# Kernel optimization log

Hardware: AMD Instinct MI355X
Metric: run time of the kernel (lower is better)

## Reference

```python
import jax, jax.numpy as jnp
import numpy as np

D = 64  # max disparity search range (d in the torch module)


def setup_inputs() -> dict:
    key = jax.random.key(0)
    k1, k2 = jax.random.split(key)
    B, C, H, W = 8, 128, 128, 256
    x1 = jax.random.normal(k1, (B, C, H, W), dtype=jnp.float32)
    x2 = jax.random.normal(k2, (B, C, H, W), dtype=jnp.float32)
    return {"x1": x1, "x2": x2}


def _corr_volume(x1, x2, d):
    # result[n, i, h, w] = (1/C) * sum_c x1[n,c,h,w] * x2[n,c,h,w-i], zero where w-i < 0
    n, c, h, w = x2.shape
    slices = []
    for i in range(d + 1):
        # shift x2 right by i columns, zero-padding on the left
        shifted = jnp.pad(x2[:, :, :, : w - i] if i > 0 else x2,
                          ((0, 0), (0, 0), (0, 0), (i, 0)))
        slices.append(jnp.sum(x1 * shifted, axis=1))  # [n, h, w]
    cv = jnp.stack(slices, axis=1)  # [n, d+1, h, w]
    return cv * (1.0 / c)


def reference(x1, x2):
    return _corr_volume(x1, x2, D)
```

## Files before the change

### kernel.cpp

```cpp
#include <hip/hip_runtime.h>
#include <hip/hip_fp16.h>


constexpr int B   = 8;
constexpr int C   = 128;
constexpr int H   = 128;
constexpr int W   = 256;
constexpr int NI  = 65;
constexpr int HW  = H * W;
constexpr int CHW = C * HW;
constexpr int KC2 = 8;
constexpr int X2W = 320;
constexpr int NCHUNK = C / (2 * KC2);

typedef _Float16 half2v __attribute__((ext_vector_type(2)));

__device__ inline unsigned int pack2(float a, float b) {
    __half2 h = __floats2half2_rn(a, b);
    return __builtin_bit_cast(unsigned int, h);
}

__device__ inline float fdot2f(unsigned int a, unsigned int b, float c) {
#if __has_builtin(__builtin_amdgcn_fdot2)
    return __builtin_amdgcn_fdot2(__builtin_bit_cast(half2v, a),
                                  __builtin_bit_cast(half2v, b), c, false);
#else
    __half2 ha = __builtin_bit_cast(__half2, a);
    __half2 hb = __builtin_bit_cast(__half2, b);
    float2 fa = __half22float2(ha), fb = __half22float2(hb);
    return fmaf(fa.x, fb.x, fmaf(fa.y, fb.y, c));
#endif
}

__global__ __launch_bounds__(512, 4)
void corr_volume_kernel(const float* __restrict__ x1,
                        const float* __restrict__ x2,
                        float* __restrict__ out) {
    const int bh  = blockIdx.x;
    const int n   = blockIdx.y;
    const int tid = threadIdx.x;
    const int l   = tid & 63;
    const int q   = tid >> 6;
    const int hsel = q >> 2;
    const int qi   = q & 3;

    __shared__ unsigned int x1h[2][KC2][W];
    __shared__ unsigned int x2h[2][KC2][X2W];

    float acc[16][4];
    #pragma unroll
    for (int il = 0; il < 16; ++il)
        #pragma unroll
        for (int wl = 0; wl < 4; ++wl) acc[il][wl] = 0.0f;
    float acc64[4] = {0.f, 0.f, 0.f, 0.f};

    const int j0a = 4 * l - 16 * qi + 48;

    const float* x1b = x1 + n * CHW + (2 * bh) * W;
    const float* x2b = x2 + n * CHW + (2 * bh) * W;

    if (tid < 256) {
        const int hh = tid >> 7;
        const int r  = (tid >> 4) & 7;
        const int cq = tid & 15;
        *(uint4*)&x2h[hh][r][4 * cq] = make_uint4(0u, 0u, 0u, 0u);
    }

    for (int t = 0; t < NCHUNK; ++t) {
        const int c0 = t * 2 * KC2;

        if (t) __syncthreads();

        {
            const int r = q;
            #pragma unroll
            for (int in2 = 0; in2 < 2; ++in2) {
                const float* gb = in2 ? x2b : x1b;
                #pragma unroll
                for (int hh = 0; hh < 2; ++hh) {
                    const float* g = gb + hh * W + (c0 + 2 * r) * HW + 4 * l;
                    const float4 lo = *(const float4*)g;
                    const float4 hi = *(const float4*)(g + HW);
                    uint4 p;
                    p.x = pack2(lo.x, hi.x); p.y = pack2(lo.y, hi.y);
                    p.z = pack2(lo.z, hi.z); p.w = pack2(lo.w, hi.w);
                    if (in2) *(uint4*)&x2h[hh][r][64 + 4 * l] = p;
                    else     *(uint4*)&x1h[hh][r][4 * l]      = p;
                }
            }
        }
        __syncthreads();

        #pragma unroll 1
        for (int c2 = 0; c2 < KC2; ++c2) {
            const uint4 a4 = *(const uint4*)&x1h[hsel][c2][4 * l];
            const unsigned int aw[4] = {a4.x, a4.y, a4.z, a4.w};
            const uint4 b0 = *(const uint4*)&x2h[hsel][c2][j0a];
            const uint4 b1 = *(const uint4*)&x2h[hsel][c2][j0a + 4];
            const uint4 b2 = *(const uint4*)&x2h[hsel][c2][j0a + 8];
            const uint4 b3 = *(const uint4*)&x2h[hsel][c2][j0a + 12];
            const uint4 b4 = *(const uint4*)&x2h[hsel][c2][j0a + 16];
            const unsigned int bw[20] = {b0.x, b0.y, b0.z, b0.w,
                                         b1.x, b1.y, b1.z, b1.w,
                                         b2.x, b2.y, b2.z, b2.w,
                                         b3.x, b3.y, b3.z, b3.w,
                                         b4.x, b4.y, b4.z, b4.w};
            #pragma unroll
            for (int il = 0; il < 16; ++il)
                #pragma unroll
                for (int wl = 0; wl < 4; ++wl)
                    acc[il][wl] = fdot2f(aw[wl], bw[16 + wl - il], acc[il][wl]);

            if (qi == 3) {
                #pragma unroll
                for (int wl = 0; wl < 4; ++wl)
                    acc64[wl] = fdot2f(aw[wl], bw[wl], acc64[wl]);
            }
        }
    }

    const float scale = 1.0f / (float)C;
    const int h = 2 * bh + hsel;
    float* outg = out + n * (NI * HW) + h * W + 4 * l;
    #pragma unroll
    for (int il = 0; il < 16; ++il) {
        const int i = 16 * qi + il;
        *(float4*)(outg + i * HW) =
            make_float4(acc[il][0] * scale, acc[il][1] * scale,
                        acc[il][2] * scale, acc[il][3] * scale);
    }
    if (qi == 3) {
        *(float4*)(outg + 64 * HW) =
            make_float4(acc64[0] * scale, acc64[1] * scale,
                        acc64[2] * scale, acc64[3] * scale);
    }
}

extern "C" void kernel_launch(void* const* d_in, const int* in_sizes, int n_in,
                              void* d_out, int out_size, void* d_ws, size_t ws_size,
                              hipStream_t stream) {
    const float* x1 = (const float*)d_in[0];
    const float* x2 = (const float*)d_in[1];
    float* out = (float*)d_out;
    dim3 grid(H / 2, B);
    corr_volume_kernel<<<grid, 512, 0, stream>>>(x1, x2, out);
}
```

Measured before the change: 308.3 us.

## Double-buffer x2 tiles with register prefetch, one row per 256-thread block

Each block now handles a single image row with 256 threads instead of two rows with 512. The x2 channel chunk is double-buffered in shared memory, and the next chunk's global loads are issued into registers before the current chunk's compute, then written to LDS afterwards, saving one barrier per chunk. x1 is read straight from global memory into registers instead of being staged in LDS. This hides load latency and cuts shared memory use, at the cost of more blocks, uncoalesced-reuse-free x1 global reads inside the inner loop, and changed occupancy bounds.

```diff
diff --git a/kernel.cpp b/kernel.cpp
--- a/kernel.cpp
+++ b/kernel.cpp
@@ -32,19 +32,16 @@
 #endif
 }
 
-__global__ __launch_bounds__(512, 4)
+__global__ __launch_bounds__(256, 3)
 void corr_volume_kernel(const float* __restrict__ x1,
                         const float* __restrict__ x2,
                         float* __restrict__ out) {
-    const int bh  = blockIdx.x;
+    const int h   = blockIdx.x;
     const int n   = blockIdx.y;
     const int tid = threadIdx.x;
     const int l   = tid & 63;
-    const int q   = tid >> 6;
-    const int hsel = q >> 2;
-    const int qi   = q & 3;
+    const int qi  = tid >> 6;
 
-    __shared__ unsigned int x1h[2][KC2][W];
     __shared__ unsigned int x2h[2][KC2][X2W];
 
     float acc[16][4];
@@ -56,50 +53,61 @@
 
     const int j0a = 4 * l - 16 * qi + 48;
 
-    const float* x1b = x1 + n * CHW + (2 * bh) * W;
-    const float* x2b = x2 + n * CHW + (2 * bh) * W;
+    const float* x1g = x1 + n * CHW + h * W;
+    const float* x2g = x2 + n * CHW + h * W;
 
-    if (tid < 256) {
-        const int hh = tid >> 7;
-        const int r  = (tid >> 4) & 7;
-        const int cq = tid & 15;
-        *(uint4*)&x2h[hh][r][4 * cq] = make_uint4(0u, 0u, 0u, 0u);
+    {
+        const int bufi = tid >> 7;
+        const int r    = (tid >> 4) & 7;
+        const int cq   = tid & 15;
+        *(uint4*)&x2h[bufi][r][4 * cq] = make_uint4(0u, 0u, 0u, 0u);
     }
 
+    float4 L[4];
+    auto issue = [&](int c0) {
+        #pragma unroll
+        for (int rr = 0; rr < 2; ++rr) {
+            const int r = 2 * qi + rr;
+            const float* g = x2g + (c0 + 2 * r) * HW + 4 * l;
+            L[2 * rr + 0] = *(const float4*)g;
+            L[2 * rr + 1] = *(const float4*)(g + HW);
+        }
+    };
+    auto commit = [&](int bufi) {
+        #pragma unroll
+        for (int rr = 0; rr < 2; ++rr) {
+            const int r = 2 * qi + rr;
+            uint4 p;
+            p.x = pack2(L[2 * rr].x, L[2 * rr + 1].x);
+            p.y = pack2(L[2 * rr].y, L[2 * rr + 1].y);
+            p.z = pack2(L[2 * rr].z, L[2 * rr + 1].z);
+            p.w = pack2(L[2 * rr].w, L[2 * rr + 1].w);
+            *(uint4*)&x2h[bufi][r][64 + 4 * l] = p;
+        }
+    };
+
+    issue(0);
+    commit(0);
+    __syncthreads();
+
     for (int t = 0; t < NCHUNK; ++t) {
-        const int c0 = t * 2 * KC2;
+        const int cur = t & 1;
+        const int c0  = t * 2 * KC2;
 
-        if (t) __syncthreads();
+        if (t + 1 < NCHUNK) issue((t + 1) * 2 * KC2);
+        asm volatile("" ::: "memory");
 
-        {
-            const int r = q;
-            #pragma unroll
-            for (int in2 = 0; in2 < 2; ++in2) {
-                const float* gb = in2 ? x2b : x1b;
-                #pragma unroll
-                for (int hh = 0; hh < 2; ++hh) {
-                    const float* g = gb + hh * W + (c0 + 2 * r) * HW + 4 * l;
-                    const float4 lo = *(const float4*)g;
-                    const float4 hi = *(const float4*)(g + HW);
-                    uint4 p;
-                    p.x = pack2(lo.x, hi.x); p.y = pack2(lo.y, hi.y);
-                    p.z = pack2(lo.z, hi.z); p.w = pack2(lo.w, hi.w);
-                    if (in2) *(uint4*)&x2h[hh][r][64 + 4 * l] = p;
-                    else     *(uint4*)&x1h[hh][r][4 * l]      = p;
-                }
-            }
-        }
-        __syncthreads();
-
-        #pragma unroll 1
+        #pragma unroll 2
         for (int c2 = 0; c2 < KC2; ++c2) {
-            const uint4 a4 = *(const uint4*)&x1h[hsel][c2][4 * l];
-            const unsigned int aw[4] = {a4.x, a4.y, a4.z, a4.w};
-            const uint4 b0 = *(const uint4*)&x2h[hsel][c2][j0a];
-            const uint4 b1 = *(const uint4*)&x2h[hsel][c2][j0a + 4];
-            const uint4 b2 = *(const uint4*)&x2h[hsel][c2][j0a + 8];
-            const uint4 b3 = *(const uint4*)&x2h[hsel][c2][j0a + 12];
-            const uint4 b4 = *(const uint4*)&x2h[hsel][c2][j0a + 16];
+            const float4 lo = *(const float4*)(x1g + (c0 + 2 * c2) * HW + 4 * l);
+            const float4 hi = *(const float4*)(x1g + (c0 + 2 * c2 + 1) * HW + 4 * l);
+            const unsigned int aw[4] = {pack2(lo.x, hi.x), pack2(lo.y, hi.y),
+                                        pack2(lo.z, hi.z), pack2(lo.w, hi.w)};
+            const uint4 b0 = *(const uint4*)&x2h[cur][c2][j0a];
+            const uint4 b1 = *(const uint4*)&x2h[cur][c2][j0a + 4];
+            const uint4 b2 = *(const uint4*)&x2h[cur][c2][j0a + 8];
+            const uint4 b3 = *(const uint4*)&x2h[cur][c2][j0a + 12];
+            const uint4 b4 = *(const uint4*)&x2h[cur][c2][j0a + 16];
             const unsigned int bw[20] = {b0.x, b0.y, b0.z, b0.w,
                                          b1.x, b1.y, b1.z, b1.w,
                                          b2.x, b2.y, b2.z, b2.w,
@@ -117,10 +125,14 @@
                     acc64[wl] = fdot2f(aw[wl], bw[wl], acc64[wl]);
             }
         }
+
+        if (t + 1 < NCHUNK) {
+            commit((t + 1) & 1);
+            __syncthreads();
+        }
     }
 
     const float scale = 1.0f / (float)C;
-    const int h = 2 * bh + hsel;
     float* outg = out + n * (NI * HW) + h * W + 4 * l;
     #pragma unroll
     for (int il = 0; il < 16; ++il) {
@@ -142,6 +154,6 @@
     const float* x1 = (const float*)d_in[0];
     const float* x2 = (const float*)d_in[1];
     float* out = (float*)d_out;
-    dim3 grid(H / 2, B);
-    corr_volume_kernel<<<grid, 512, 0, stream>>>(x1, x2, out);
+    dim3 grid(H, B);
+    corr_volume_kernel<<<grid, 256, 0, stream>>>(x1, x2, out);
 }
```

Result: slower. 333.0 us (+8.0%).
